# Kernel optimization log

Measured on AMD Instinct MI355X. Metric: run time of the kernel, lower is better.

Reference implementation:

```python
import jax, jax.numpy as jnp
import numpy as np

N_NODES = 50000
N_EDGES = 800000
IN_CH, HID_CH, OUT_CH = 256, 128, 64


def setup_inputs() -> dict:
    key = jax.random.key(0)
    k1, k2, k3, k4 = jax.random.split(key, 4)
    x = jax.random.normal(k1, (N_NODES, IN_CH), dtype=jnp.float32)
    edge_index = jax.random.randint(k2, (2, N_EDGES), 0, N_NODES, dtype=jnp.int64)
    # Glorot-style init for the GCN weight matrices, zero bias (PyG default)
    W1 = jax.random.normal(k3, (IN_CH, HID_CH), dtype=jnp.float32) * (1.0 / np.sqrt(IN_CH))
    b1 = jnp.zeros((HID_CH,), dtype=jnp.float32)
    W2 = jax.random.normal(k4, (HID_CH, OUT_CH), dtype=jnp.float32) * (1.0 / np.sqrt(HID_CH))
    b2 = jnp.zeros((OUT_CH,), dtype=jnp.float32)
    return {"x": x, "edge_index": edge_index, "W1": W1, "b1": b1, "W2": W2, "b2": b2}


def _gcn_conv(x, W, b, src, dst, dinv_sqrt, n_nodes):
    # linear transform then degree-normalized scatter-add aggregation
    h = x @ W                                        # [N, F_out]
    norm = dinv_sqrt[src] * dinv_sqrt[dst]           # [E+N]
    msg = h[src] * norm[:, None]                     # gather + scale
    out = jax.ops.segment_sum(msg, dst, num_segments=n_nodes)
    return out + b


def reference(x, edge_index, W1, b1, W2, b2):
    n_nodes = x.shape[0]
    loops = jnp.arange(n_nodes, dtype=edge_index.dtype)
    src = jnp.concatenate([edge_index[0], loops])    # add self-loops (PyG default)
    dst = jnp.concatenate([edge_index[1], loops])
    # symmetric normalization: deg computed over targets incl. self-loops
    deg = jax.ops.segment_sum(jnp.ones_like(dst, dtype=x.dtype), dst, num_segments=n_nodes)
    dinv_sqrt = jnp.where(deg > 0, jax.lax.rsqrt(deg), 0.0)
    h = jax.nn.relu(_gcn_conv(x, W1, b1, src, dst, dinv_sqrt, n_nodes))
    return _gcn_conv(h, W2, b2, src, dst, dinv_sqrt, n_nodes)
```

## Files before the change

### kernel.cpp

```cpp
#include <hip/hip_runtime.h>


typedef __attribute__((ext_vector_type(4))) float floatx4;
typedef _Float16 __attribute__((ext_vector_type(8))) half8v;

#define BUCK_SH 6
#define BUCK    64
#define NBLK    256

#define AS1(p) ((const __attribute__((address_space(1))) void*)(p))
#define AS3(p) ((__attribute__((address_space(3))) void*)(p))

__global__ void detect64_kernel(const int* __restrict__ ei, int* __restrict__ flag) {
    __shared__ int nz;
    if (threadIdx.x == 0) nz = 0;
    __syncthreads();
    if (ei[2 * threadIdx.x + 1] != 0) atomicOr(&nz, 1);
    __syncthreads();
    if (threadIdx.x == 0) *flag = (nz == 0) ? 1 : 0;
}

__device__ __forceinline__ int edge_id(const int* __restrict__ ei, int is64, long long pos) {
    return is64 ? ei[2 * pos] : ei[(int)pos];
}

__global__ void hist2_kernel(const int* __restrict__ ei, const int* __restrict__ flag,
                             int* __restrict__ hist2, int E, int NB, int chunk) {
    __shared__ int h[1024];
    const int t = threadIdx.x;
    for (int i = t; i < NB; i += blockDim.x) h[i] = 0;
    __syncthreads();
    const int is64 = *flag;
    const int lo = blockIdx.x * chunk;
    const int hi = min(E, lo + chunk);
    for (int e = lo + t; e < hi; e += blockDim.x) {
        int d = edge_id(ei, is64, (long long)E + e);
        atomicAdd(&h[d >> BUCK_SH], 1);
    }
    __syncthreads();
    for (int i = t; i < NB; i += blockDim.x) hist2[(long long)blockIdx.x * NB + i] = h[i];
}

__global__ void bscan2_kernel(const int* __restrict__ hist2, int* __restrict__ bbase,
                              int* __restrict__ start2, int NB, int E) {
    __shared__ int sm[1024];
    const int t = threadIdx.x;
    int col = 0;
    if (t < NB)
        for (int b = 0; b < NBLK; ++b) col += hist2[(long long)b * NB + t];
    sm[t] = col;
    __syncthreads();
    for (int s = 1; s < 1024; s <<= 1) {
        int u = (t >= s) ? sm[t - s] : 0;
        __syncthreads();
        sm[t] += u;
        __syncthreads();
    }
    int excl = sm[t] - col;
    if (t < NB) {
        bbase[t] = excl;
        int run = excl;
        for (int b = 0; b < NBLK; ++b) {
            start2[(long long)b * NB + t] = run;
            run += hist2[(long long)b * NB + t];
        }
    }
    if (t == 0) bbase[NB] = E;
}

__global__ void scatter2_kernel(const int* __restrict__ ei, const int* __restrict__ flag,
                                const int* __restrict__ start2, unsigned* __restrict__ ebuf,
                                int E, int NB, int chunk) {
    __shared__ int hcur[1024];
    const int t = threadIdx.x;
    for (int i = t; i < NB; i += blockDim.x)
        hcur[i] = start2[(long long)blockIdx.x * NB + i];
    __syncthreads();
    const int is64 = *flag;
    const int lo = blockIdx.x * chunk;
    const int hi = min(E, lo + chunk);
    for (int e = lo + t; e < hi; e += blockDim.x) {
        int s = edge_id(ei, is64, e);
        int d = edge_id(ei, is64, (long long)E + e);
        int pos = atomicAdd(&hcur[d >> BUCK_SH], 1);
        ebuf[pos] = (unsigned)s | ((unsigned)(d & (BUCK - 1)) << 26);
    }
}

__global__ void csrbuild_kernel(const unsigned* __restrict__ ebuf, const int* __restrict__ bbase,
                                int* __restrict__ offs, float* __restrict__ dinv,
                                int* __restrict__ csr, int N, int NB, int E) {
    __shared__ int cnt[BUCK], exc[BUCK], cur[BUCK];
    const int b = blockIdx.x;
    const int t = threadIdx.x;
    if (t < BUCK) { cnt[t] = 0; cur[t] = 0; }
    __syncthreads();
    const int lo = bbase[b], hi = bbase[b + 1];
    for (int i = lo + t; i < hi; i += blockDim.x)
        atomicAdd(&cnt[ebuf[i] >> 26], 1);
    __syncthreads();
    if (t == 0) {
        int run = 0;
        for (int l = 0; l < BUCK; ++l) { exc[l] = run; run += cnt[l]; }
    }
    __syncthreads();
    if (t < BUCK) {
        int n = b * BUCK + t;
        if (n < N) {
            offs[n] = lo + exc[t];
            dinv[n] = rsqrtf(1.0f + (float)cnt[t]);
        }
    }
    if (b == NB - 1 && t == 0) offs[N] = E;
    for (int i = lo + t; i < hi; i += blockDim.x) {
        unsigned e = ebuf[i];
        int l = e >> 26;
        int p = lo + exc[l] + atomicAdd(&cur[l], 1);
        csr[p] = (int)(e & 0x03FFFFFFu);
    }
}

__device__ __forceinline__ void convW_one(const float* W, _Float16* Wt, int K, int Nc, int idx) {
    if (idx >= K * Nc) return;
    int k = idx / Nc, n = idx % Nc;
    Wt[(long long)n * K + k] = (_Float16)W[idx];
}

__global__ void convW_kernel(const float* __restrict__ W1, _Float16* __restrict__ T1,
                             int K1, int N1, int nb1,
                             const float* __restrict__ W2, _Float16* __restrict__ T2,
                             int K2, int N2) {
    if ((int)blockIdx.x < nb1) {
        convW_one(W1, T1, K1, N1, blockIdx.x * blockDim.x + threadIdx.x);
    } else {
        convW_one(W2, T2, K2, N2, (blockIdx.x - nb1) * blockDim.x + threadIdx.x);
    }
}

template <int NCOL, int K>
__launch_bounds__(256)
__global__ void gemm_f16_kernel(const float* __restrict__ A,
                                const _Float16* __restrict__ Bt,
                                _Float16* __restrict__ C, int M) {
    constexpr int NCB = NCOL / 16;
    constexpr int BM = 128, BK = 64;
    constexpr int NC = K / BK;
    constexpr int UNITS = BM * BK / 4;
    __shared__ float As[2][BM * BK];

    const int tid  = threadIdx.x;
    const int wave = tid >> 6;
    const int lane = tid & 63;
    const int n15  = lane & 15;
    const int q    = lane >> 4;
    const int row0 = blockIdx.x * BM;

    floatx4 acc[2][NCB];
#pragma unroll
    for (int rt = 0; rt < 2; ++rt)
#pragma unroll
        for (int c = 0; c < NCB; ++c) acc[rt][c] = (floatx4){0.f, 0.f, 0.f, 0.f};

    auto stage = [&](int buf, int kc) {
#pragma unroll
        for (int j = 0; j < UNITS / 256; ++j) {
            int g = j * 256 + tid;
            int r = g >> 4;
            int u = (g & 15) ^ (r & 15);
            int gr = row0 + r;
            if (gr >= M) gr = M - 1;
            const float* gp = &A[(long long)gr * K + kc + u * 4];
            float* lp = &As[buf][g * 4];
            __builtin_amdgcn_global_load_lds(AS1(gp), AS3(lp), 16, 0, 0);
        }
    };

    stage(0, 0);
    __syncthreads();

#pragma unroll
    for (int c = 0; c < NC; ++c) {
        if (c + 1 < NC) stage((c + 1) & 1, (c + 1) * BK);
        const int buf = c & 1;
#pragma unroll
        for (int ks = 0; ks < 2; ++ks) {
            half8v af[2];
#pragma unroll
            for (int rt = 0; rt < 2; ++rt) {
                const int R = wave * 32 + rt * 16 + n15;
                const int u0 = ks * 8 + q * 2;
                const int p0 = (u0)     ^ (R & 15);
                const int p1 = (u0 + 1) ^ (R & 15);
                float4 f0 = *(const float4*)&As[buf][R * BK + p0 * 4];
                float4 f1 = *(const float4*)&As[buf][R * BK + p1 * 4];
                af[rt][0] = (_Float16)f0.x; af[rt][1] = (_Float16)f0.y;
                af[rt][2] = (_Float16)f0.z; af[rt][3] = (_Float16)f0.w;
                af[rt][4] = (_Float16)f1.x; af[rt][5] = (_Float16)f1.y;
                af[rt][6] = (_Float16)f1.z; af[rt][7] = (_Float16)f1.w;
            }
#pragma unroll
            for (int cb = 0; cb < NCB; ++cb) {
                const _Float16* bp = &Bt[(long long)(cb * 16 + n15) * K + c * BK + ks * 32 + q * 8];
                half8v bf = *(const half8v*)bp;
                acc[0][cb] = __builtin_amdgcn_mfma_f32_16x16x32_f16(af[0], bf, acc[0][cb], 0, 0, 0);
                acc[1][cb] = __builtin_amdgcn_mfma_f32_16x16x32_f16(af[1], bf, acc[1][cb], 0, 0, 0);
            }
        }
        if (c + 1 < NC) __syncthreads();
    }

#pragma unroll
    for (int rt = 0; rt < 2; ++rt) {
#pragma unroll
        for (int cb = 0; cb < NCB; ++cb) {
            int col = cb * 16 + n15;
#pragma unroll
            for (int r = 0; r < 4; ++r) {
                int gr = row0 + wave * 32 + rt * 16 + q * 4 + r;
                if (gr < M) C[(long long)gr * NCOL + col] = (_Float16)acc[rt][cb][r];
            }
        }
    }
}

template <int F, int RELU>
__launch_bounds__(256)
__global__ void gatherh_kernel(const _Float16* __restrict__ h, const int* __restrict__ csr,
                               const int* __restrict__ offs, const float* __restrict__ dinv,
                               const float* __restrict__ bias, float* __restrict__ out, int N) {
    constexpr int L = F / 8;
    constexpr int NPB = 256 / L;
    const int n = blockIdx.x * NPB + threadIdx.x / L;
    const int c8 = (threadIdx.x % L) * 8;
    if (n >= N) return;

    const float di = dinv[n];
    half8v hs = *(const half8v*)&h[(long long)n * F + c8];
    float acc[8];
    const float sd = di * di;
#pragma unroll
    for (int j = 0; j < 8; ++j) acc[j] = (float)hs[j] * sd;

    int j = offs[n];
    const int end = offs[n + 1];
    for (; j + 7 < end; j += 8) {
        int s[8];
        float ws[8];
        half8v v[8];
#pragma unroll
        for (int u = 0; u < 8; ++u) s[u] = csr[j + u];
#pragma unroll
        for (int u = 0; u < 8; ++u) ws[u] = dinv[s[u]];
#pragma unroll
        for (int u = 0; u < 8; ++u) v[u] = *(const half8v*)&h[(long long)s[u] * F + c8];
#pragma unroll
        for (int u = 0; u < 8; ++u) {
            float w = ws[u] * di;
#pragma unroll
            for (int t = 0; t < 8; ++t) acc[t] = fmaf((float)v[u][t], w, acc[t]);
        }
    }
    for (; j < end; ++j) {
        int s = csr[j];
        float w = dinv[s] * di;
        half8v v = *(const half8v*)&h[(long long)s * F + c8];
#pragma unroll
        for (int t = 0; t < 8; ++t) acc[t] = fmaf((float)v[t], w, acc[t]);
    }

    float4 b0 = *(const float4*)&bias[c8];
    float4 b1 = *(const float4*)&bias[c8 + 4];
    float bb[8] = {b0.x, b0.y, b0.z, b0.w, b1.x, b1.y, b1.z, b1.w};
#pragma unroll
    for (int t = 0; t < 8; ++t) {
        acc[t] += bb[t];
        if (RELU) acc[t] = fmaxf(acc[t], 0.f);
    }
    float* o = &out[(long long)n * F + c8];
    *(float4*)o       = make_float4(acc[0], acc[1], acc[2], acc[3]);
    *(float4*)(o + 4) = make_float4(acc[4], acc[5], acc[6], acc[7]);
}

extern "C" void kernel_launch(void* const* d_in, const int* in_sizes, int n_in,
                              void* d_out, int out_size, void* d_ws, size_t ws_size,
                              hipStream_t stream) {
    const float* x  = (const float*)d_in[0];
    const int*   ei = (const int*)d_in[1];
    const float* W1 = (const float*)d_in[2];
    const float* b1 = (const float*)d_in[3];
    const float* W2 = (const float*)d_in[4];
    const float* b2 = (const float*)d_in[5];
    float* out = (float*)d_out;

    const int IN_CH = 256, HID = 128, OUT = 64;
    const int N = in_sizes[0] / IN_CH;
    const int E = in_sizes[1] / 2;
    const int NB = (N + BUCK - 1) / BUCK;
    const int chunk = (E + NBLK - 1) / NBLK;

    char* w = (char*)d_ws;
    size_t off_b = 0;
    auto alloc = [&](size_t bytes) { void* p = w + off_b; off_b = (off_b + bytes + 255) & ~(size_t)255; return p; };
    int*   flag   = (int*)alloc(256);
    int*   hist2  = (int*)alloc((size_t)NBLK * NB * 4);
    int*   start2 = (int*)alloc((size_t)NBLK * NB * 4);
    int*   bbase  = (int*)alloc((size_t)(NB + 1) * 4);
    int*   offs   = (int*)alloc((size_t)(N + 1) * 4);
    float* dinv   = (float*)alloc((size_t)N * 4);
    unsigned* ebuf = (unsigned*)alloc((size_t)E * 4);
    int*   csr    = (int*)alloc((size_t)E * 4);
    _Float16* W1t = (_Float16*)alloc((size_t)IN_CH * HID * 2);
    _Float16* W2t = (_Float16*)alloc((size_t)HID * OUT * 2);
    _Float16* h1  = (_Float16*)alloc((size_t)N * HID * 2);
    float* agg1   = (float*)alloc((size_t)N * HID * 4);
    _Float16* h2  = h1;

    const int T = 256;
    detect64_kernel<<<1, 256, 0, stream>>>(ei, flag);
    hist2_kernel<<<NBLK, T, 0, stream>>>(ei, flag, hist2, E, NB, chunk);
    bscan2_kernel<<<1, 1024, 0, stream>>>(hist2, bbase, start2, NB, E);
    scatter2_kernel<<<NBLK, T, 0, stream>>>(ei, flag, start2, ebuf, E, NB, chunk);
    csrbuild_kernel<<<NB, T, 0, stream>>>(ebuf, bbase, offs, dinv, csr, N, NB, E);

    {
        int nb1 = (IN_CH * HID + T - 1) / T;
        int nb2 = (HID * OUT + T - 1) / T;
        convW_kernel<<<nb1 + nb2, T, 0, stream>>>(W1, W1t, IN_CH, HID, nb1,
                                                  W2, W2t, HID, OUT);
    }

    gemm_f16_kernel<128, 256><<<(N + 127) / 128, 256, 0, stream>>>(x, W1t, h1, N);
    gatherh_kernel<128, 1><<<(N * 16 + 255) / 256, 256, 0, stream>>>(h1, csr, offs, dinv, b1, agg1, N);
    gemm_f16_kernel<64, 128><<<(N + 127) / 128, 256, 0, stream>>>(agg1, W2t, h2, N);
    gatherh_kernel<64, 0><<<(N * 8 + 255) / 256, 256, 0, stream>>>(h2, csr, offs, dinv, b2, out, N);
}
```

Measured before the change: 242.1 us.

## Store GEMM output in 32-column panels and gather per panel; parallelize bucket scan

The GEMM epilogue now writes h in column-panel-major layout (32 fp16 columns, 64 bytes per row per panel). Aggregation then runs as several launches, one per panel, so each pass's random-gather working set (N x 64 bytes) is small enough to stay in cache. Separately, the single-block bucket scan is split into a multi-block per-column scan with transposed start offsets plus a small base scan. The trade-off is that CSR, offsets and dinv are re-read once per panel, and there are more kernel launches.

```diff
diff --git a/kernel.cpp b/kernel.cpp
--- a/kernel.cpp
+++ b/kernel.cpp
@@ -41,14 +41,25 @@
     for (int i = t; i < NB; i += blockDim.x) hist2[(long long)blockIdx.x * NB + i] = h[i];
 }
 
-__global__ void bscan2_kernel(const int* __restrict__ hist2, int* __restrict__ bbase,
-                              int* __restrict__ start2, int NB, int E) {
+__global__ void colscan_kernel(const int* __restrict__ hist2, int* __restrict__ start2t,
+                               int* __restrict__ colsum, int NB) {
+    int t = blockIdx.x * blockDim.x + threadIdx.x;
+    if (t >= NB) return;
+    int run = 0;
+    for (int b = 0; b < NBLK; ++b) {
+        int v = hist2[(long long)b * NB + t];
+        start2t[(long long)t * NBLK + b] = run;
+        run += v;
+    }
+    colsum[t] = run;
+}
+
+__global__ void basescan_kernel(const int* __restrict__ colsum, int* __restrict__ bbase,
+                                int NB, int E) {
     __shared__ int sm[1024];
     const int t = threadIdx.x;
-    int col = 0;
-    if (t < NB)
-        for (int b = 0; b < NBLK; ++b) col += hist2[(long long)b * NB + t];
-    sm[t] = col;
+    int v = (t < NB) ? colsum[t] : 0;
+    sm[t] = v;
     __syncthreads();
     for (int s = 1; s < 1024; s <<= 1) {
         int u = (t >= s) ? sm[t - s] : 0;
@@ -56,25 +67,17 @@
         sm[t] += u;
         __syncthreads();
     }
-    int excl = sm[t] - col;
-    if (t < NB) {
-        bbase[t] = excl;
-        int run = excl;
-        for (int b = 0; b < NBLK; ++b) {
-            start2[(long long)b * NB + t] = run;
-            run += hist2[(long long)b * NB + t];
-        }
-    }
+    if (t < NB) bbase[t] = sm[t] - v;
     if (t == 0) bbase[NB] = E;
 }
 
 __global__ void scatter2_kernel(const int* __restrict__ ei, const int* __restrict__ flag,
-                                const int* __restrict__ start2, unsigned* __restrict__ ebuf,
-                                int E, int NB, int chunk) {
+                                const int* __restrict__ bbase, const int* __restrict__ start2t,
+                                unsigned* __restrict__ ebuf, int E, int NB, int chunk) {
     __shared__ int hcur[1024];
     const int t = threadIdx.x;
     for (int i = t; i < NB; i += blockDim.x)
-        hcur[i] = start2[(long long)blockIdx.x * NB + i];
+        hcur[i] = bbase[i] + start2t[(long long)i * NBLK + blockIdx.x];
     __syncthreads();
     const int is64 = *flag;
     const int lo = blockIdx.x * chunk;
@@ -214,28 +217,28 @@
 #pragma unroll
         for (int cb = 0; cb < NCB; ++cb) {
             int col = cb * 16 + n15;
+            long long pbase = (long long)(col >> 5) * M * 32 + (col & 31);
 #pragma unroll
             for (int r = 0; r < 4; ++r) {
                 int gr = row0 + wave * 32 + rt * 16 + q * 4 + r;
-                if (gr < M) C[(long long)gr * NCOL + col] = (_Float16)acc[rt][cb][r];
+                if (gr < M) C[pbase + (long long)gr * 32] = (_Float16)acc[rt][cb][r];
             }
         }
     }
 }
 
-template <int F, int RELU>
+template <int RELU>
 __launch_bounds__(256)
-__global__ void gatherh_kernel(const _Float16* __restrict__ h, const int* __restrict__ csr,
+__global__ void gatherq_kernel(const _Float16* __restrict__ hq, const int* __restrict__ csr,
                                const int* __restrict__ offs, const float* __restrict__ dinv,
-                               const float* __restrict__ bias, float* __restrict__ out, int N) {
-    constexpr int L = F / 8;
-    constexpr int NPB = 256 / L;
-    const int n = blockIdx.x * NPB + threadIdx.x / L;
-    const int c8 = (threadIdx.x % L) * 8;
+                               const float* __restrict__ bias, float* __restrict__ outp,
+                               int ostride, int N) {
+    const int n = blockIdx.x * 64 + (threadIdx.x >> 2);
+    const int c8 = (threadIdx.x & 3) * 8;
     if (n >= N) return;
 
     const float di = dinv[n];
-    half8v hs = *(const half8v*)&h[(long long)n * F + c8];
+    half8v hs = *(const half8v*)&hq[(long long)n * 32 + c8];
     float acc[8];
     const float sd = di * di;
 #pragma unroll
@@ -252,7 +255,7 @@
 #pragma unroll
         for (int u = 0; u < 8; ++u) ws[u] = dinv[s[u]];
 #pragma unroll
-        for (int u = 0; u < 8; ++u) v[u] = *(const half8v*)&h[(long long)s[u] * F + c8];
+        for (int u = 0; u < 8; ++u) v[u] = *(const half8v*)&hq[(long long)s[u] * 32 + c8];
 #pragma unroll
         for (int u = 0; u < 8; ++u) {
             float w = ws[u] * di;
@@ -263,7 +266,7 @@
     for (; j < end; ++j) {
         int s = csr[j];
         float w = dinv[s] * di;
-        half8v v = *(const half8v*)&h[(long long)s * F + c8];
+        half8v v = *(const half8v*)&hq[(long long)s * 32 + c8];
 #pragma unroll
         for (int t = 0; t < 8; ++t) acc[t] = fmaf((float)v[t], w, acc[t]);
     }
@@ -276,7 +279,7 @@
         acc[t] += bb[t];
         if (RELU) acc[t] = fmaxf(acc[t], 0.f);
     }
-    float* o = &out[(long long)n * F + c8];
+    float* o = &outp[(long long)n * ostride + c8];
     *(float4*)o       = make_float4(acc[0], acc[1], acc[2], acc[3]);
     *(float4*)(o + 4) = make_float4(acc[4], acc[5], acc[6], acc[7]);
 }
@@ -301,25 +304,27 @@
     char* w = (char*)d_ws;
     size_t off_b = 0;
     auto alloc = [&](size_t bytes) { void* p = w + off_b; off_b = (off_b + bytes + 255) & ~(size_t)255; return p; };
-    int*   flag   = (int*)alloc(256);
-    int*   hist2  = (int*)alloc((size_t)NBLK * NB * 4);
-    int*   start2 = (int*)alloc((size_t)NBLK * NB * 4);
-    int*   bbase  = (int*)alloc((size_t)(NB + 1) * 4);
-    int*   offs   = (int*)alloc((size_t)(N + 1) * 4);
-    float* dinv   = (float*)alloc((size_t)N * 4);
+    int*   flag    = (int*)alloc(256);
+    int*   hist2   = (int*)alloc((size_t)NBLK * NB * 4);
+    int*   start2t = (int*)alloc((size_t)NB * NBLK * 4);
+    int*   colsum  = (int*)alloc((size_t)NB * 4);
+    int*   bbase   = (int*)alloc((size_t)(NB + 1) * 4);
+    int*   offs    = (int*)alloc((size_t)(N + 1) * 4);
+    float* dinv    = (float*)alloc((size_t)N * 4);
     unsigned* ebuf = (unsigned*)alloc((size_t)E * 4);
-    int*   csr    = (int*)alloc((size_t)E * 4);
-    _Float16* W1t = (_Float16*)alloc((size_t)IN_CH * HID * 2);
-    _Float16* W2t = (_Float16*)alloc((size_t)HID * OUT * 2);
-    _Float16* h1  = (_Float16*)alloc((size_t)N * HID * 2);
-    float* agg1   = (float*)alloc((size_t)N * HID * 4);
-    _Float16* h2  = h1;
+    int*   csr     = (int*)alloc((size_t)E * 4);
+    _Float16* W1t  = (_Float16*)alloc((size_t)IN_CH * HID * 2);
+    _Float16* W2t  = (_Float16*)alloc((size_t)HID * OUT * 2);
+    _Float16* h1   = (_Float16*)alloc((size_t)N * HID * 2);
+    float* agg1    = (float*)alloc((size_t)N * HID * 4);
+    _Float16* h2   = h1;
 
     const int T = 256;
     detect64_kernel<<<1, 256, 0, stream>>>(ei, flag);
     hist2_kernel<<<NBLK, T, 0, stream>>>(ei, flag, hist2, E, NB, chunk);
-    bscan2_kernel<<<1, 1024, 0, stream>>>(hist2, bbase, start2, NB, E);
-    scatter2_kernel<<<NBLK, T, 0, stream>>>(ei, flag, start2, ebuf, E, NB, chunk);
+    colscan_kernel<<<(NB + T - 1) / T, T, 0, stream>>>(hist2, start2t, colsum, NB);
+    basescan_kernel<<<1, 1024, 0, stream>>>(colsum, bbase, NB, E);
+    scatter2_kernel<<<NBLK, T, 0, stream>>>(ei, flag, bbase, start2t, ebuf, E, NB, chunk);
     csrbuild_kernel<<<NB, T, 0, stream>>>(ebuf, bbase, offs, dinv, csr, N, NB, E);
 
     {
@@ -329,8 +334,18 @@
                                                   W2, W2t, HID, OUT);
     }
 
+    const int gblocks = (N + 63) / 64;
+
     gemm_f16_kernel<128, 256><<<(N + 127) / 128, 256, 0, stream>>>(x, W1t, h1, N);
-    gatherh_kernel<128, 1><<<(N * 16 + 255) / 256, 256, 0, stream>>>(h1, csr, offs, dinv, b1, agg1, N);
+    for (int q = 0; q < 4; ++q) {
+        gatherq_kernel<1><<<gblocks, 256, 0, stream>>>(
+            h1 + (size_t)q * N * 32, csr, offs, dinv, b1 + q * 32,
+            agg1 + q * 32, HID, N);
+    }
     gemm_f16_kernel<64, 128><<<(N + 127) / 128, 256, 0, stream>>>(agg1, W2t, h2, N);
-    gatherh_kernel<64, 0><<<(N * 8 + 255) / 256, 256, 0, stream>>>(h2, csr, offs, dinv, b2, out, N);
-}
+    for (int q = 0; q < 2; ++q) {
+        gatherq_kernel<0><<<gblocks, 256, 0, stream>>>(
+            h2 + (size_t)q * N * 32, csr, offs, dinv, b2 + q * 32,
+            out + q * 32, OUT, N);
+    }
+}
```

Result: slower. 276.7 us (+14.3%).
